# Performance work log

Hardware: AMD Instinct MI355X
Metric: run time of the kernel (lower is better)

## Reference

```python
import jax, jax.numpy as jnp
import numpy as np

BN_EPS = 1e-5
STRIDE = 12          # ACCENT_DOWNSAMPLE_STRIDE
NQ = 8               # ACCENT_VQ_QUANTIZERS
K = 256              # ACCENT_VQ_CODEBOOK_SIZE
VQ_D = 16            # ACCENT_VQ_DIM
EMB = 128            # ACCENT_EMBEDDING_DIM


def conv1d(x, w, b, stride=1, padding=0):
    # x: (B, Cin, T), w: (Cout, Cin, Kw)
    y = jax.lax.conv_general_dilated(
        x, w, window_strides=(stride,), padding=[(padding, padding)],
        dimension_numbers=("NCW", "OIW", "NCW"))
    return y + b[None, :, None]


def batchnorm(x, gamma, beta, mean, var):
    # eval-mode BatchNorm1d over channel dim
    inv = jax.lax.rsqrt(var + BN_EPS)
    return (x - mean[None, :, None]) * (inv * gamma)[None, :, None] + beta[None, :, None]


def setup_inputs() -> dict:
    key = jax.random.key(0)
    ks = jax.random.split(key, 12)
    C = 256
    d = {
        "mel_spectrogram": jax.random.normal(ks[0], (16, 80, 4096), jnp.float32),
        "w1": jax.random.normal(ks[1], (C, 80, 5), jnp.float32) * 0.05,
        "b1": jnp.zeros((C,), jnp.float32),
        "g1": jnp.ones((C,), jnp.float32),
        "be1": jnp.zeros((C,), jnp.float32),
        "m1": jax.random.normal(ks[2], (C,), jnp.float32) * 0.1,
        "v1": jax.random.uniform(ks[3], (C,), jnp.float32, 0.5, 1.5),
        "w2": jax.random.normal(ks[4], (C, C, 5), jnp.float32) * 0.03,
        "b2": jnp.zeros((C,), jnp.float32),
        "g2": jnp.ones((C,), jnp.float32),
        "be2": jnp.zeros((C,), jnp.float32),
        "m2": jax.random.normal(ks[5], (C,), jnp.float32) * 0.1,
        "v2": jax.random.uniform(ks[6], (C,), jnp.float32, 0.5, 1.5),
        "wd": jax.random.normal(ks[7], (EMB, C, 2 * STRIDE), jnp.float32) * 0.02,
        "bd": jnp.zeros((EMB,), jnp.float32),
        "wp": jax.random.normal(ks[8], (VQ_D, EMB, 1), jnp.float32) * 0.1,
        "bp": jnp.zeros((VQ_D,), jnp.float32),
        "codebooks": jax.random.normal(ks[9], (NQ, K, VQ_D), jnp.float32) * 0.3,
    }
    return d


def reference(mel_spectrogram, w1, b1, g1, be1, m1, v1,
              w2, b2, g2, be2, m2, v2, wd, bd, wp, bp, codebooks):
    # CNN stack
    x = jax.nn.relu(batchnorm(conv1d(mel_spectrogram, w1, b1, 1, 2), g1, be1, m1, v1))
    x = jax.nn.relu(batchnorm(conv1d(x, w2, b2, 1, 2), g2, be2, m2, v2))
    # Downsample conv: kernel=24, stride=12, pad=6
    e_a_unq = conv1d(x, wd, bd, STRIDE, STRIDE // 2)          # (B, 128, T')
    z = conv1d(e_a_unq, wp, bp, 1, 0)                          # (B, 16, T')
    # RVQ: 8 sequential cdist-argmin-subtract steps
    r = jnp.transpose(z, (0, 2, 1))                            # (B, T', 16)
    idx_list = []
    for q in range(NQ):
        cb = codebooks[q]                                      # (K, 16)
        # squared euclidean distances (B, T', K)
        d = (jnp.sum(r * r, -1, keepdims=True)
             - 2.0 * jnp.einsum("btd,kd->btk", r, cb)
             + jnp.sum(cb * cb, -1))
        idx = jnp.argmin(d, axis=-1)                           # (B, T')
        idx_list.append(idx)
        r = r - cb[idx]                                        # residual update
    indices = jnp.stack(idx_list, axis=0)                      # (NQ, B, T')
    return e_a_unq, indices
```

## Files before the change

kernel.cpp:

```cpp
#include <hip/hip_runtime.h>
#include <math.h>

#define B_    16
#define T_    4096
#define C_    256
#define CIN1  80
#define EMB   128
#define TP    341
#define NPOS  (B_*TP)
#define NQ_   8
#define KCB   256
#define BN_EPS 1e-5

__global__ __launch_bounds__(256) void prep_common(
    const float* __restrict__ wd,
    const float* __restrict__ b1, const float* __restrict__ g1,
    const float* __restrict__ be1, const float* __restrict__ m1,
    const float* __restrict__ v1,
    const float* __restrict__ b2, const float* __restrict__ g2,
    const float* __restrict__ be2, const float* __restrict__ m2,
    const float* __restrict__ v2,
    float* __restrict__ wdt,
    double* __restrict__ a1, double* __restrict__ bt1,
    double* __restrict__ a2, double* __restrict__ bt2)
{
    int j = blockIdx.x * 256 + threadIdx.x;
    if (j < 256*24*128) wdt[j] = wd[(size_t)(j & 127) * 6144 + (j >> 7)];
    if (j < 256) {
        double inv1 = 1.0 / sqrt((double)v1[j] + BN_EPS);
        double s1 = (double)g1[j] * inv1;
        a1[j]  = s1;
        bt1[j] = ((double)b1[j] - (double)m1[j]) * s1 + (double)be1[j];
        double inv2 = 1.0 / sqrt((double)v2[j] + BN_EPS);
        double s2 = (double)g2[j] * inv2;
        a2[j]  = s2;
        bt2[j] = ((double)b2[j] - (double)m2[j]) * s2 + (double)be2[j];
    }
}

__global__ __launch_bounds__(256) void prep_wf64(
    const float* __restrict__ w1, const float* __restrict__ w2,
    double* __restrict__ w1td, double* __restrict__ w2td)
{
    int j = blockIdx.x * 256 + threadIdx.x;
    if (j < 256*5*256) w2td[j] = (double)w2[(size_t)(j & 255) * 1280 + (j >> 8)];
    if (j < 80*5*256)  w1td[j] = (double)w1[(size_t)(j & 255) * 400 + (j >> 8)];
}
__global__ __launch_bounds__(256) void prep_wf32(
    const float* __restrict__ w1, const float* __restrict__ w2,
    float* __restrict__ w1tf, float* __restrict__ w2tf)
{
    int j = blockIdx.x * 256 + threadIdx.x;
    if (j < 256*5*256) w2tf[j] = w2[(size_t)(j & 255) * 1280 + (j >> 8)];
    if (j < 80*5*256)  w1tf[j] = w1[(size_t)(j & 255) * 400 + (j >> 8)];
}

__device__ __forceinline__ int swz_pair(int col) {
    int bw = col >> 1;
    return ((bw ^ ((bw >> 3) & 7)) << 1);
}
__device__ __forceinline__ int swz_scalar(int col) {
    int bw = col >> 1;
    return (((bw ^ ((bw >> 3) & 7)) << 1) | (col & 1));
}

template<int CIN, typename Tin, typename WT>
__global__ __launch_bounds__(256, 4) void conv5_v10(
    const Tin* __restrict__ in,
    const WT* __restrict__ wt,
    const double* __restrict__ alpha, const double* __restrict__ beta,
    double* __restrict__ out)
{
    const int b  = blockIdx.z;
    const int t0 = blockIdx.y * 128;
    const int wv = __builtin_amdgcn_readfirstlane((int)(threadIdx.x >> 6));
    const int lane = threadIdx.x & 63;
    const int co0 = blockIdx.x * 64 + wv * 16;
    const int t = t0 + lane * 2;

    double acc[16][2];
    #pragma unroll
    for (int c = 0; c < 16; ++c) { acc[c][0] = 0.0; acc[c][1] = 0.0; }

    const Tin* xb = in + (size_t)b * CIN * T_;
    const bool interior = (t0 != 0) && (t0 + 130 <= T_);

    for (int ci = 0; ci < CIN; ++ci) {
        double xv[6];
        const Tin* xp = xb + (size_t)ci * T_ + (t - 2);
        if (interior) {
            #pragma unroll
            for (int d = 0; d < 6; ++d) xv[d] = (double)xp[d];
        } else {
            #pragma unroll
            for (int d = 0; d < 6; ++d) {
                int tt = t - 2 + d;
                xv[d] = (tt >= 0 && tt < T_) ? (double)xp[d] : 0.0;
            }
        }
        const WT* wrow = wt + (size_t)ci * 5 * 256 + co0;
        #pragma unroll
        for (int k = 0; k < 5; ++k) {
            #pragma unroll
            for (int c = 0; c < 16; ++c) {
                double w = (double)wrow[k * 256 + c];
                acc[c][0] = fma(w, xv[k],     acc[c][0]);
                acc[c][1] = fma(w, xv[k + 1], acc[c][1]);
            }
        }
    }

    #pragma unroll
    for (int c = 0; c < 16; ++c) {
        int co = co0 + c;
        double a = alpha[co], bt = beta[co];
        double y0 = fma(acc[c][0], a, bt);
        double y1 = fma(acc[c][1], a, bt);
        double2 o;
        o.x = y0 > 0.0 ? y0 : 0.0;
        o.y = y1 > 0.0 ? y1 : 0.0;
        *(double2*)&out[((size_t)(b * C_ + co)) * T_ + t] = o;
    }
}

__global__ __launch_bounds__(256, 2) void convd_f64_v7(
    const double* __restrict__ x2,
    const float* __restrict__ wdt,
    double* __restrict__ parts,
    int nb, int nsplit, int cis)
{
    const int bz  = blockIdx.z;
    const int s   = bz % nsplit;
    const int b   = bz / nsplit;
    const int tp0 = blockIdx.x * 128;
    const int tid = threadIdx.x;
    const int tcol = tid & 15;
    const int crow = tid >> 4;

    __shared__ __align__(16) double xs2[24][132];
    __shared__ __align__(16) double wsh[24][128];

    double acc[8][8];
    #pragma unroll
    for (int i = 0; i < 8; ++i)
        #pragma unroll
        for (int j = 0; j < 8; ++j) acc[i][j] = 0.0;

    const int tbase = tp0 * 12 - 6;
    const int ci_begin = s * cis;

    for (int c = ci_begin; c < ci_begin + cis; ++c) {
        for (int i = tid; i < 1548; i += 256) {
            int t = tbase + i;
            double v = (t >= 0 && t < T_)
                ? x2[((size_t)(b * 256 + c)) * T_ + t] : 0.0;
            int tp = (i * 43691) >> 19;
            int kp = i - tp * 12;
            xs2[kp][swz_scalar(tp)] = v;
            if (tp >= 1) xs2[kp + 12][swz_scalar(tp - 1)] = v;
        }
        for (int i = tid; i < 24 * 128; i += 256) {
            int r = i >> 7, cc = i & 127;
            wsh[r][cc] = (double)wdt[((size_t)c * 24 + r) * 128 + cc];
        }
        __syncthreads();

        #pragma unroll 4
        for (int k = 0; k < 24; ++k) {
            double wv[8];
            #pragma unroll
            for (int m = 0; m < 4; ++m) {
                double2 w2v = *(const double2*)&wsh[k][crow * 8 + 2 * m];
                wv[2 * m] = w2v.x; wv[2 * m + 1] = w2v.y;
            }
            #pragma unroll
            for (int jp = 0; jp < 4; ++jp) {
                double2 xp = *(const double2*)&xs2[k][swz_pair(tcol * 2 + 32 * jp)];
                #pragma unroll
                for (int i = 0; i < 8; ++i) {
                    acc[i][jp * 2]     = fma(wv[i], xp.x, acc[i][jp * 2]);
                    acc[i][jp * 2 + 1] = fma(wv[i], xp.y, acc[i][jp * 2 + 1]);
                }
            }
        }
        __syncthreads();
    }

    #pragma unroll
    for (int i = 0; i < 8; ++i) {
        int co = crow * 8 + i;
        #pragma unroll
        for (int jp = 0; jp < 4; ++jp) {
            #pragma unroll
            for (int e = 0; e < 2; ++e) {
                int tp = tp0 + tcol * 2 + 32 * jp + e;
                if (tp < TP)
                    parts[(((size_t)s * nb + b) * EMB + co) * TP + tp] = acc[i][jp * 2 + e];
            }
        }
    }
}

__global__ __launch_bounds__(256) void convd_combine(
    double* __restrict__ parts,
    const float* __restrict__ bd,
    float* __restrict__ e_out,
    int nb, int b_off, int nsplit)
{
    int idx = blockIdx.x * 256 + threadIdx.x;
    int total = nb * EMB * TP;
    if (idx >= total) return;
    int rem = idx % (EMB * TP);
    int co = rem / TP;
    size_t stride = (size_t)nb * EMB * TP;
    double y = 0.0;
    for (int s = 0; s < nsplit; ++s)
        y += parts[(size_t)s * stride + idx];
    y += (double)bd[co];
    parts[idx] = y;
    e_out[(size_t)b_off * EMB * TP + idx] = (float)y;
}

__global__ __launch_bounds__(128) void zproj_f64(
    const double* __restrict__ ed,
    const float* __restrict__ wp,
    const float* __restrict__ bp,
    double* __restrict__ z)
{
    const int b = blockIdx.y;
    const int t = blockIdx.x * 128 + threadIdx.x;
    __shared__ double wps[16][128];
    for (int i = threadIdx.x; i < 16 * 128; i += 128)
        wps[i >> 7][i & 127] = (double)wp[i];
    __syncthreads();
    if (t >= TP) return;
    double acc[16];
    #pragma unroll
    for (int v = 0; v < 16; ++v) acc[v] = (double)bp[v];
    for (int co = 0; co < 128; ++co) {
        double x = ed[((size_t)(b * EMB + co)) * TP + t];
        #pragma unroll
        for (int v = 0; v < 16; ++v) acc[v] = fma(x, wps[v][co], acc[v]);
    }
    #pragma unroll
    for (int v = 0; v < 16; ++v)
        z[((size_t)(b * TP + t)) * 16 + v] = acc[v];
}

__global__ __launch_bounds__(256) void rvq_f64_v2(
    const double* __restrict__ z,
    const float* __restrict__ cb,
    float* __restrict__ out_idx)
{
    const int pos = blockIdx.x;
    const int tid = threadIdx.x;
    const int lane = tid & 63;
    const int wv = tid >> 6;

    __shared__ double r[16];
    __shared__ double wd_s[4];
    __shared__ int wi_s[4];
    __shared__ int best_s;

    if (tid < 16) r[tid] = z[(size_t)pos * 16 + tid];
    __syncthreads();

    for (int q = 0; q < NQ_; ++q) {
        const float* c = cb + ((size_t)(q * KCB) + tid) * 16;
        double d = 0.0;
        #pragma unroll
        for (int i = 0; i < 16; ++i) {
            double diff = r[i] - (double)c[i];
            d = fma(diff, diff, d);
        }
        int idx = tid;
        #pragma unroll
        for (int sft = 32; sft > 0; sft >>= 1) {
            double d2 = __shfl_down(d, sft, 64);
            int i2 = __shfl_down(idx, sft, 64);
            if (d2 < d || (d2 == d && i2 < idx)) { d = d2; idx = i2; }
        }
        if (lane == 0) { wd_s[wv] = d; wi_s[wv] = idx; }
        __syncthreads();
        if (tid == 0) {
            double bd_ = wd_s[0]; int bi = wi_s[0];
            #pragma unroll
            for (int w = 1; w < 4; ++w) {
                if (wd_s[w] < bd_ || (wd_s[w] == bd_ && wi_s[w] < bi)) {
                    bd_ = wd_s[w]; bi = wi_s[w];
                }
            }
            best_s = bi;
            out_idx[(size_t)q * NPOS + pos] = (float)bi;
        }
        __syncthreads();
        int best = best_s;
        if (tid < 16)
            r[tid] = r[tid] - (double)cb[((size_t)(q * KCB) + best) * 16 + tid];
        __syncthreads();
    }
}

extern "C" void kernel_launch(void* const* d_in, const int* in_sizes, int n_in,
                              void* d_out, int out_size, void* d_ws, size_t ws_size,
                              hipStream_t stream) {
    const float* mel = (const float*)d_in[0];
    const float* w1  = (const float*)d_in[1];
    const float* b1  = (const float*)d_in[2];
    const float* g1  = (const float*)d_in[3];
    const float* be1 = (const float*)d_in[4];
    const float* m1  = (const float*)d_in[5];
    const float* v1  = (const float*)d_in[6];
    const float* w2  = (const float*)d_in[7];
    const float* b2  = (const float*)d_in[8];
    const float* g2  = (const float*)d_in[9];
    const float* be2 = (const float*)d_in[10];
    const float* m2  = (const float*)d_in[11];
    const float* v2  = (const float*)d_in[12];
    const float* wd  = (const float*)d_in[13];
    const float* bd  = (const float*)d_in[14];
    const float* wp  = (const float*)d_in[15];
    const float* bp  = (const float*)d_in[16];
    const float* cb  = (const float*)d_in[17];

    const int nb = 8;
    const int ngrp = B_ / nb;
    const int nsplit = 16;
    const int cis = 256 / nsplit;

    const size_t x1_bytes = (size_t)nb * C_ * T_ * 8;
    const size_t x2_bytes = (size_t)nb * C_ * T_ * 8;
    const size_t zd_bytes = (size_t)B_ * TP * 16 * 8;

    const size_t needA = x1_bytes + x2_bytes + (size_t)80*5*256*8
                       + (size_t)256*5*256*8 + (size_t)256*24*128*4
                       + 4*2048 + zd_bytes + 8192;
    const bool tierA = (ws_size >= needA);

    char* ws = (char*)d_ws;
    size_t off = 0;
    auto alloc = [&](size_t bytes) -> char* {
        char* p = ws + off;
        off = (off + bytes + 255) & ~(size_t)255;
        return p;
    };
    char* shared = alloc(x1_bytes);
    double* x1d  = (double*)shared;
    double* parts= (double*)shared;
    double* x2d  = (double*)alloc(x2_bytes);
    void*   w1t  = (void*)alloc(tierA ? (size_t)80*5*256*8  : (size_t)80*5*256*4);
    void*   w2t  = (void*)alloc(tierA ? (size_t)256*5*256*8 : (size_t)256*5*256*4);
    float*  wdt  = (float*)alloc((size_t)256*24*128*4);
    double* a1d  = (double*)alloc(2048);
    double* bt1d = (double*)alloc(2048);
    double* a2d  = (double*)alloc(2048);
    double* bt2d = (double*)alloc(2048);
    double* zd   = (double*)alloc(zd_bytes);

    float* e_out   = (float*)d_out;
    float* idx_out = (float*)d_out + (size_t)B_ * EMB * TP;

    prep_common<<<3072, 256, 0, stream>>>(wd, b1, g1, be1, m1, v1,
                                          b2, g2, be2, m2, v2,
                                          wdt, a1d, bt1d, a2d, bt2d);
    if (tierA)
        prep_wf64<<<1280, 256, 0, stream>>>(w1, w2, (double*)w1t, (double*)w2t);
    else
        prep_wf32<<<1280, 256, 0, stream>>>(w1, w2, (float*)w1t, (float*)w2t);

    const int comb_blocks = (nb * EMB * TP + 255) / 256;
    for (int g = 0; g < ngrp; ++g) {
        const float* mel_g = mel + (size_t)(g * nb) * CIN1 * T_;
        if (tierA) {
            conv5_v10<CIN1, float, double><<<dim3(4, 32, nb), 256, 0, stream>>>(
                mel_g, (const double*)w1t, a1d, bt1d, x1d);
            conv5_v10<C_, double, double><<<dim3(4, 32, nb), 256, 0, stream>>>(
                x1d, (const double*)w2t, a2d, bt2d, x2d);
        } else {
            conv5_v10<CIN1, float, float><<<dim3(4, 32, nb), 256, 0, stream>>>(
                mel_g, (const float*)w1t, a1d, bt1d, x1d);
            conv5_v10<C_, double, float><<<dim3(4, 32, nb), 256, 0, stream>>>(
                x1d, (const float*)w2t, a2d, bt2d, x2d);
        }
        convd_f64_v7<<<dim3(3, 1, nb * nsplit), 256, 0, stream>>>(
            x2d, wdt, parts, nb, nsplit, cis);
        convd_combine<<<comb_blocks, 256, 0, stream>>>(
            parts, bd, e_out, nb, g * nb, nsplit);
        zproj_f64<<<dim3(3, nb), 128, 0, stream>>>(
            parts, wp, bp, zd + (size_t)g * nb * TP * 16);
    }
    rvq_f64_v2<<<NPOS, 256, 0, stream>>>(zd, cb, idx_out);
}
```

Baseline: 1.926 ms.

## Double-buffer input loads and remap conv5 blocks for XCD-aware locality

The conv5 kernel now unrolls the input-channel loop by two and prefetches the next channel's six input values into a second register buffer while the FMAs for the current channel run, so global-load latency is hidden. The 3D grid becomes a 1D grid with a block-id remap that groups the four output-channel tiles of each (batch, time) tile at a stride of 8. The apparent aim is to have blocks that share the same input slice land on the same XCD and reuse its L2. The extra register buffer adds register pressure under launch_bounds(256,4).

Measured after the change: 2.181 ms. 13.3% more time.

```diff
diff --git a/kernel.cpp b/kernel.cpp
--- a/kernel.cpp
+++ b/kernel.cpp
@@ -65,50 +65,74 @@
 }
 
 template<int CIN, typename Tin, typename WT>
-__global__ __launch_bounds__(256, 4) void conv5_v10(
+__global__ __launch_bounds__(256, 4) void conv5_v11(
     const Tin* __restrict__ in,
     const WT* __restrict__ wt,
     const double* __restrict__ alpha, const double* __restrict__ beta,
     double* __restrict__ out)
 {
-    const int b  = blockIdx.z;
-    const int t0 = blockIdx.y * 128;
+    const int id  = blockIdx.x;
+    const int low = id & 7;
+    const int hi  = id >> 3;
+    const int cot = hi & 3;
+    const int g   = ((hi >> 2) << 3) | low;
+    const int b   = g >> 5;
+    const int t0  = (g & 31) * 128;
+
     const int wv = __builtin_amdgcn_readfirstlane((int)(threadIdx.x >> 6));
     const int lane = threadIdx.x & 63;
-    const int co0 = blockIdx.x * 64 + wv * 16;
+    const int co0 = cot * 64 + wv * 16;
     const int t = t0 + lane * 2;
 
     double acc[16][2];
     #pragma unroll
     for (int c = 0; c < 16; ++c) { acc[c][0] = 0.0; acc[c][1] = 0.0; }
 
-    const Tin* xb = in + (size_t)b * CIN * T_;
+    const Tin* xb = in + (size_t)b * CIN * T_ + (t - 2);
     const bool interior = (t0 != 0) && (t0 + 130 <= T_);
 
-    for (int ci = 0; ci < CIN; ++ci) {
-        double xv[6];
-        const Tin* xp = xb + (size_t)ci * T_ + (t - 2);
-        if (interior) {
-            #pragma unroll
-            for (int d = 0; d < 6; ++d) xv[d] = (double)xp[d];
-        } else {
-            #pragma unroll
-            for (int d = 0; d < 6; ++d) {
-                int tt = t - 2 + d;
-                xv[d] = (tt >= 0 && tt < T_) ? (double)xp[d] : 0.0;
-            }
-        }
+    double xv0[6], xv1[6];
+    #define LOADX(CI, XV)                                                \
+        {                                                                \
+            const Tin* xp = xb + (size_t)(CI) * T_;                      \
+            if (interior) {                                              \
+                _Pragma("unroll")                                        \
+                for (int d = 0; d < 6; ++d) XV[d] = (double)xp[d];       \
+            } else {                                                     \
+                _Pragma("unroll")                                        \
+                for (int d = 0; d < 6; ++d) {                            \
+                    int tt = t - 2 + d;                                  \
+                    XV[d] = (tt >= 0 && tt < T_) ? (double)xp[d] : 0.0;  \
+                }                                                        \
+            }                                                            \
+        }
+
+    LOADX(0, xv0);
+    for (int ci = 0; ci < CIN; ci += 2) {
+        LOADX(ci + 1, xv1);
         const WT* wrow = wt + (size_t)ci * 5 * 256 + co0;
         #pragma unroll
         for (int k = 0; k < 5; ++k) {
             #pragma unroll
             for (int c = 0; c < 16; ++c) {
                 double w = (double)wrow[k * 256 + c];
-                acc[c][0] = fma(w, xv[k],     acc[c][0]);
-                acc[c][1] = fma(w, xv[k + 1], acc[c][1]);
-            }
-        }
-    }
+                acc[c][0] = fma(w, xv0[k],     acc[c][0]);
+                acc[c][1] = fma(w, xv0[k + 1], acc[c][1]);
+            }
+        }
+        if (ci + 2 < CIN) LOADX(ci + 2, xv0);
+        wrow += 5 * 256;
+        #pragma unroll
+        for (int k = 0; k < 5; ++k) {
+            #pragma unroll
+            for (int c = 0; c < 16; ++c) {
+                double w = (double)wrow[k * 256 + c];
+                acc[c][0] = fma(w, xv1[k],     acc[c][0]);
+                acc[c][1] = fma(w, xv1[k + 1], acc[c][1]);
+            }
+        }
+    }
+    #undef LOADX
 
     #pragma unroll
     for (int c = 0; c < 16; ++c) {
@@ -369,17 +393,18 @@
         prep_wf32<<<1280, 256, 0, stream>>>(w1, w2, (float*)w1t, (float*)w2t);
 
     const int comb_blocks = (nb * EMB * TP + 255) / 256;
+    const int conv_blocks = 4 * 32 * nb;
     for (int g = 0; g < ngrp; ++g) {
         const float* mel_g = mel + (size_t)(g * nb) * CIN1 * T_;
         if (tierA) {
-            conv5_v10<CIN1, float, double><<<dim3(4, 32, nb), 256, 0, stream>>>(
+            conv5_v11<CIN1, float, double><<<conv_blocks, 256, 0, stream>>>(
                 mel_g, (const double*)w1t, a1d, bt1d, x1d);
-            conv5_v10<C_, double, double><<<dim3(4, 32, nb), 256, 0, stream>>>(
+            conv5_v11<C_, double, double><<<conv_blocks, 256, 0, stream>>>(
                 x1d, (const double*)w2t, a2d, bt2d, x2d);
         } else {
-            conv5_v10<CIN1, float, float><<<dim3(4, 32, nb), 256, 0, stream>>>(
+            conv5_v11<CIN1, float, float><<<conv_blocks, 256, 0, stream>>>(
                 mel_g, (const float*)w1t, a1d, bt1d, x1d);
-            conv5_v10<C_, double, float><<<dim3(4, 32, nb), 256, 0, stream>>>(
+            conv5_v11<C_, double, float><<<conv_blocks, 256, 0, stream>>>(
                 x1d, (const float*)w2t, a2d, bt2d, x2d);
         }
         convd_f64_v7<<<dim3(3, 1, nb * nsplit), 256, 0, stream>>>(
```
